# Kernel tuning notes

Hardware: AMD Instinct MI355X
Metric: run time of the kernel (lower is better)

The kernel has to match this reference:

```python
import jax, jax.numpy as jnp
import numpy as np

NEG_INF = float('-inf')

def setup_inputs() -> dict:
    key = jax.random.key(0)
    k1, k2 = jax.random.split(key)
    B, T, S, H, D = 2, 2048, 2048, 8, 64
    q = jax.random.normal(k1, (B, T, H, D), dtype=jnp.float32)
    kv = jax.random.normal(k2, (B, S, 2, H, D), dtype=jnp.float32)
    key_padding_mask = jnp.ones((B, S), dtype=bool)  # True = valid key
    return {"q": q, "kv": kv, "key_padding_mask": key_padding_mask, "causal": 1}


def reference(q, kv, key_padding_mask, causal):
    # q: (B,T,H,D), kv: (B,S,2,H,D)
    k = kv[:, :, 0]  # (B,S,H,D)
    v = kv[:, :, 1]  # (B,S,H,D)
    D = q.shape[-1]
    scale = D ** (-0.5)
    # scores: (B,H,T,S)
    scores = jnp.einsum('bthd,bshd->bhts', q, k) * scale
    # mask: True means "mask out" (matches torch masked_fill semantics)
    mask = ~key_padding_mask[:, None, None, :]  # (B,1,1,S)
    if causal:
        T, S = scores.shape[2], scores.shape[3]
        causal_mask = jnp.triu(jnp.ones((T, S), dtype=bool), k=1)  # (T,S)
        mask = mask | causal_mask[None, None, :, :]
    scores = jnp.where(mask, NEG_INF, scores)
    attn = jax.nn.softmax(scores, axis=-1)
    out = jnp.einsum('bhts,bshd->bthd', attn, v)  # (B,T,H,D)
    return out
```

## Files before the change

### kernel.cpp

```cpp
#include <hip/hip_runtime.h>
#include <hip/hip_bf16.h>

typedef __bf16 bf8_t __attribute__((ext_vector_type(8)));
typedef float  f4_t  __attribute__((ext_vector_type(4)));

constexpr int Bc = 2;
constexpr int Tc = 2048;
constexpr int Sc = 2048;
constexpr int Hc = 8;
constexpr int Dc = 64;
constexpr int BQ = 64;
constexpr int BK = 32;
constexpr int nQB = Tc / BQ;
constexpr int NKT = Sc / BK;
constexpr int NP  = nQB / 2;
constexpr int NS  = 4;
constexpr int TILE_H = 4096;
constexpr int KH = 2048;
constexpr int KTH = 4096;
constexpr int LDP = BK + 4;

__device__ __forceinline__ void g2l16(const void* g, void* l) {
    __builtin_amdgcn_global_load_lds(
        (const __attribute__((address_space(1))) void*)g,
        (__attribute__((address_space(3))) void*)l, 16, 0, 0);
}

__global__ __launch_bounds__(256)
void fa_prep(const float* __restrict__ kv, const int* __restrict__ kpm,
             __bf16* __restrict__ kvb, unsigned* __restrict__ kpmw)
{
    const int idx    = blockIdx.x * 256 + threadIdx.x;
    const int tile   = idx >> 9;
    const int within = idx & 511;
    const int b  = tile >> 9;
    const int h  = (tile >> 6) & 7;
    const int s0 = (tile & 63) * BK;
    __bf16* dst = kvb + (size_t)tile * TILE_H + within * 8;
    bf8_t o;
    if (within < 256) {
        const int row = within >> 3;
        const int col = ((within & 7) * 8) ^ ((row & 7) << 3);
        const float* src = kv + (((size_t)(b * Sc + s0 + row) * 2 + 0) * Hc + h) * Dc + col;
        const float4 x0 = *(const float4*)src;
        const float4 x1 = *(const float4*)(src + 4);
        o[0] = (__bf16)x0.x; o[1] = (__bf16)x0.y; o[2] = (__bf16)x0.z; o[3] = (__bf16)x0.w;
        o[4] = (__bf16)x1.x; o[5] = (__bf16)x1.y; o[6] = (__bf16)x1.z; o[7] = (__bf16)x1.w;
    } else {
        const int c    = within - 256;
        const int vrow = c >> 2;
        const int sc   = (c & 3) * 8;
        const float* src = kv + (((size_t)(b * Sc + s0 + sc) * 2 + 1) * Hc + h) * Dc + vrow;
        #pragma unroll
        for (int j = 0; j < 8; ++j) o[j] = (__bf16)src[(size_t)j * 2 * Hc * Dc];
    }
    *(bf8_t*)dst = o;

    if (idx < Bc * NKT) {
        const int bb = idx >> 6, tt = idx & 63;
        unsigned m = 0;
        for (int k = 0; k < 32; ++k)
            m |= (kpm[bb * Sc + tt * BK + k] != 0 ? 1u : 0u) << k;
        kpmw[idx] = m;
    }
}

__global__ __launch_bounds__(256, 4)
void fa_part(const float* __restrict__ q,
             const __bf16* __restrict__ kvb,
             const unsigned* __restrict__ kpmw,
             const int* __restrict__ causal_p,
             float* __restrict__ part_o,
             float* __restrict__ part_l)
{
    __shared__ __bf16 shK[3 * KTH];
    __shared__ __bf16 Ps[4][16][LDP];

    const int tid  = threadIdx.x;
    const int wave = tid >> 6;
    const int lane = tid & 63;
    const int n16  = lane & 15;
    const int quad = lane >> 4;

    const int bid = blockIdx.x;
    const int h   = bid & 7;
    const int g   = bid >> 3;
    const int b   = g >> 6;
    const int rem = g & 63;
    const int p   = rem >> 2;
    const int s   = rem & 3;
    const int causal = causal_p[0];

    const int nA   = causal ? (nQB - p)  : 32;
    const int nB   = causal ? (p + 1)    : 32;
    const int ntot = nA + nB;
    const int lo   = (ntot * s + 3) >> 2;
    const int hi   = (ntot * (s + 1) + 3) >> 2;

    const __bf16* kvt = kvb + (size_t)((b * Hc + h) * NKT) * TILE_H;
    const unsigned* mw_b = kpmw + b * NKT;

    const int kA_off = n16 * 64 + ((quad * 8) ^ ((n16 & 7) << 3));
    const int lds_st = tid * 8;
    const int vOff   = n16 * 32 + quad * 8;
    const float scale = 0.125f;

    #pragma unroll 1
    for (int seg = 0; seg < 2; ++seg) {
        const int qt = seg ? p : (nQB - 1 - p);
        const int t0 = seg ? (max(lo, nA) - nA) : lo;
        const int t1 = seg ? (hi - nA)          : min(hi, nA);
        if (t0 >= t1) continue;

        __syncthreads();

        const int q_base = qt * BQ;
        const int tq     = q_base + wave * 16 + quad * 4;

        bf8_t a_q[2];
        {
            const int trow = q_base + wave * 16 + n16;
            const float* qrow = q + ((size_t)(b * Tc + trow) * Hc + h) * Dc;
            #pragma unroll
            for (int f = 0; f < 2; ++f) {
                const float4 x0 = *(const float4*)(qrow + f * 32 + quad * 8);
                const float4 x1 = *(const float4*)(qrow + f * 32 + quad * 8 + 4);
                bf8_t v;
                v[0] = (__bf16)(x0.x * scale); v[1] = (__bf16)(x0.y * scale);
                v[2] = (__bf16)(x0.z * scale); v[3] = (__bf16)(x0.w * scale);
                v[4] = (__bf16)(x1.x * scale); v[5] = (__bf16)(x1.y * scale);
                v[6] = (__bf16)(x1.z * scale); v[7] = (__bf16)(x1.w * scale);
                a_q[f] = v;
            }
        }

        f4_t o_acc[4];
        #pragma unroll
        for (int dt = 0; dt < 4; ++dt) o_acc[dt] = (f4_t){0.f, 0.f, 0.f, 0.f};
        float l_r[4] = {0.f, 0.f, 0.f, 0.f};

        int cu = 0, nx = KTH, nn = 2 * KTH;
        {
            const __bf16* src = kvt + (size_t)(2 * t0) * TILE_H;
            g2l16(src + lds_st,          &shK[lds_st]);
            g2l16(src + TILE_H + lds_st, &shK[2048 + lds_st]);
        }

        for (int it = t0; it < t1; ++it) {
            const int kb = it * 64;
            const unsigned cm0 = mw_b[2 * it];
            const unsigned cm1 = mw_b[2 * it + 1];

            const __bf16* vb0 = kvt + (size_t)(2 * it) * TILE_H + KH + vOff;
            const __bf16* vb1 = vb0 + TILE_H;
            const bf8_t bv0 = *(const bf8_t*)(vb0);
            const bf8_t bv1 = *(const bf8_t*)(vb0 + 512);
            const bf8_t bv2 = *(const bf8_t*)(vb0 + 1024);
            const bf8_t bv3 = *(const bf8_t*)(vb0 + 1536);
            const bf8_t bv4 = *(const bf8_t*)(vb1);
            const bf8_t bv5 = *(const bf8_t*)(vb1 + 512);
            const bf8_t bv6 = *(const bf8_t*)(vb1 + 1024);
            const bf8_t bv7 = *(const bf8_t*)(vb1 + 1536);

            if (it + 1 < t1) {
                const __bf16* srcn = kvt + (size_t)(2 * (it + 1)) * TILE_H;
                g2l16(srcn + lds_st,          &shK[nx + lds_st]);
                g2l16(srcn + TILE_H + lds_st, &shK[nx + 2048 + lds_st]);
                asm volatile("s_waitcnt vmcnt(10)" ::: "memory");
            } else {
                asm volatile("s_waitcnt vmcnt(8)" ::: "memory");
            }
            __builtin_amdgcn_s_barrier();

            #pragma unroll
            for (int hh = 0; hh < 2; ++hh) {
                const unsigned cmw = hh ? cm1 : cm0;
                #pragma unroll
                for (int sub = 0; sub < 2; ++sub) {
                    const int kbase = cu + hh * 2048 + sub * 1024;
                    const bf8_t bk0 = *(const bf8_t*)&shK[kbase + kA_off];
                    const bf8_t bk1 = *(const bf8_t*)&shK[kbase + (kA_off ^ 32)];
                    f4_t acc = (f4_t){0.f, 0.f, 0.f, 0.f};
                    __builtin_amdgcn_s_setprio(1);
                    acc = __builtin_amdgcn_mfma_f32_16x16x32_bf16(a_q[0], bk0, acc, 0, 0, 0);
                    acc = __builtin_amdgcn_mfma_f32_16x16x32_bf16(a_q[1], bk1, acc, 0, 0, 0);
                    __builtin_amdgcn_s_setprio(0);
                    const int key = kb + hh * 32 + sub * 16 + n16;
                    const bool kvalid = ((cmw >> (sub * 16 + n16)) & 1u) != 0;
                    #pragma unroll
                    for (int r = 0; r < 4; ++r) {
                        const bool valid = kvalid && (!causal || key <= tq + r);
                        const float pp = valid ? __expf(acc[r] - 8.0f) : 0.0f;
                        l_r[r] += pp;
                        Ps[wave][quad * 4 + r][sub * 16 + n16] = (__bf16)pp;
                    }
                }

                asm volatile("s_waitcnt lgkmcnt(0)" ::: "memory");

                const bf8_t a_p = *(const bf8_t*)&Ps[wave][n16][quad * 8];
                __builtin_amdgcn_s_setprio(1);
                if (hh == 0) {
                    o_acc[0] = __builtin_amdgcn_mfma_f32_16x16x32_bf16(a_p, bv0, o_acc[0], 0, 0, 0);
                    o_acc[1] = __builtin_amdgcn_mfma_f32_16x16x32_bf16(a_p, bv1, o_acc[1], 0, 0, 0);
                    o_acc[2] = __builtin_amdgcn_mfma_f32_16x16x32_bf16(a_p, bv2, o_acc[2], 0, 0, 0);
                    o_acc[3] = __builtin_amdgcn_mfma_f32_16x16x32_bf16(a_p, bv3, o_acc[3], 0, 0, 0);
                } else {
                    o_acc[0] = __builtin_amdgcn_mfma_f32_16x16x32_bf16(a_p, bv4, o_acc[0], 0, 0, 0);
                    o_acc[1] = __builtin_amdgcn_mfma_f32_16x16x32_bf16(a_p, bv5, o_acc[1], 0, 0, 0);
                    o_acc[2] = __builtin_amdgcn_mfma_f32_16x16x32_bf16(a_p, bv6, o_acc[2], 0, 0, 0);
                    o_acc[3] = __builtin_amdgcn_mfma_f32_16x16x32_bf16(a_p, bv7, o_acc[3], 0, 0, 0);
                }
                __builtin_amdgcn_s_setprio(0);
            }

            const int tswap = cu; cu = nx; nx = nn; nn = tswap;
        }

        #pragma unroll
        for (int off = 1; off < 16; off <<= 1) {
            #pragma unroll
            for (int r = 0; r < 4; ++r) l_r[r] += __shfl_xor(l_r[r], off, 16);
        }

        const size_t slot = (size_t)(((b * Hc + h) * NP + p) * NS + s) * 2 + seg;
        float* po = part_o + slot * (BQ * Dc);
        #pragma unroll
        for (int dt = 0; dt < 4; ++dt) {
            #pragma unroll
            for (int r = 0; r < 4; ++r) {
                const int row = wave * 16 + quad * 4 + r;
                po[row * Dc + dt * 16 + n16] = o_acc[dt][r];
            }
        }
        if (n16 == 0) {
            #pragma unroll
            for (int r = 0; r < 4; ++r) {
                const int row = wave * 16 + quad * 4 + r;
                part_l[slot * BQ + row] = l_r[r];
            }
        }
    }
}

__global__ __launch_bounds__(256, 4)
void fa_reduce(const float* __restrict__ part_o,
               const float* __restrict__ part_l,
               const int* __restrict__ causal_p,
               float* __restrict__ out)
{
    const int gtid = blockIdx.x * 256 + threadIdx.x;
    const int e    = gtid & (BQ * Dc / 4 - 1);
    const int qi   = gtid >> 10;
    const int row  = e >> 4;
    const int d4   = e & 15;

    const int qt = qi & (nQB - 1);
    const int h  = (qi >> 5) & (Hc - 1);
    const int b  = qi >> 8;
    const int causal = causal_p[0];

    const int p    = (qt < NP) ? qt : (nQB - 1 - qt);
    const int seg  = (qt < NP) ? 1 : 0;
    const int nA   = causal ? (nQB - p) : 32;
    const int nB   = causal ? (p + 1)   : 32;
    const int ntot = nA + nB;
    const int segLo = seg ? nA : 0;
    const int segHi = seg ? ntot : nA;

    float4 acc = make_float4(0.f, 0.f, 0.f, 0.f);
    float  l   = 0.f;
    #pragma unroll
    for (int s = 0; s < NS; ++s) {
        const int lo = (ntot * s + 3) >> 2;
        const int hi = (ntot * (s + 1) + 3) >> 2;
        if (lo < segHi && segLo < hi) {
            const size_t slot = (size_t)(((b * Hc + h) * NP + p) * NS + s) * 2 + seg;
            const float4 v = *(const float4*)(part_o + slot * (BQ * Dc) + row * Dc + d4 * 4);
            acc.x += v.x; acc.y += v.y; acc.z += v.z; acc.w += v.w;
            l += part_l[slot * BQ + row];
        }
    }
    const float inv = 1.0f / l;
    const int t = qt * BQ + row;
    float4 o;
    o.x = acc.x * inv; o.y = acc.y * inv; o.z = acc.z * inv; o.w = acc.w * inv;
    *(float4*)(out + ((size_t)(b * Tc + t) * Hc + h) * Dc + d4 * 4) = o;
}

extern "C" void kernel_launch(void* const* d_in, const int* in_sizes, int n_in,
                              void* d_out, int out_size, void* d_ws, size_t ws_size,
                              hipStream_t stream) {
    const float* q   = (const float*)d_in[0];
    const float* kv  = (const float*)d_in[1];
    const int*   kpm = (const int*)d_in[2];
    const int*   cz  = (const int*)d_in[3];
    float*       out = (float*)d_out;

    __bf16* kvb = (__bf16*)d_ws;
    const size_t kvb_bytes = (size_t)Bc * Hc * NKT * TILE_H * sizeof(__bf16);
    unsigned* kpmw = (unsigned*)((char*)d_ws + kvb_bytes);
    float* part_o  = (float*)((char*)d_ws + kvb_bytes + 4096);

    const size_t nslots = (size_t)Bc * Hc * NP * NS * 2;
    float* part_l = part_o + nslots * (BQ * Dc);

    const int grid0 = Bc * Hc * NKT * 512 / 256;
    fa_prep<<<grid0, 256, 0, stream>>>(kv, kpm, kvb, kpmw);

    const int grid1 = Bc * Hc * NP * NS;
    fa_part<<<grid1, 256, 0, stream>>>(q, kvb, kpmw, cz, part_o, part_l);

    const int grid2 = (int)((size_t)Bc * Hc * nQB * (BQ * Dc / 4) / 256);
    fa_reduce<<<grid2, 256, 0, stream>>>(part_o, part_l, cz, out);
}
```

Measured before the change: 111.4 us.

## Compute transposed S tile and move P to registers via ds_bpermute instead of LDS

Swaps the MFMA operand order so each lane holds scores for four consecutive keys of a single query row. P is packed to bf16 and rearranged into the A-operand layout with ds_bpermute, replacing the shared-memory Ps round-trip and its lgkmcnt wait. The row-sum reduction becomes per-lane plus cross-quad shuffles and bpermutes. The second half of the V global loads is also moved after the barrier, with the vmcnt thresholds adjusted to match. Split indexing is generalized to NS with division.

```diff
diff --git a/kernel.cpp b/kernel.cpp
--- a/kernel.cpp
+++ b/kernel.cpp
@@ -3,6 +3,7 @@
 
 typedef __bf16 bf8_t __attribute__((ext_vector_type(8)));
 typedef float  f4_t  __attribute__((ext_vector_type(4)));
+typedef int    i4_t  __attribute__((ext_vector_type(4)));
 
 constexpr int Bc = 2;
 constexpr int Tc = 2048;
@@ -18,12 +19,17 @@
 constexpr int TILE_H = 4096;
 constexpr int KH = 2048;
 constexpr int KTH = 4096;
-constexpr int LDP = BK + 4;
 
 __device__ __forceinline__ void g2l16(const void* g, void* l) {
     __builtin_amdgcn_global_load_lds(
         (const __attribute__((address_space(1))) void*)g,
         (__attribute__((address_space(3))) void*)l, 16, 0, 0);
+}
+
+__device__ __forceinline__ int pack_bf16(float lo, float hi) {
+    const unsigned l16 = (unsigned)__builtin_bit_cast(unsigned short, (__bf16)lo);
+    const unsigned h16 = (unsigned)__builtin_bit_cast(unsigned short, (__bf16)hi);
+    return (int)(l16 | (h16 << 16));
 }
 
 __global__ __launch_bounds__(256)
@@ -74,7 +80,6 @@
              float* __restrict__ part_l)
 {
     __shared__ __bf16 shK[3 * KTH];
-    __shared__ __bf16 Ps[4][16][LDP];
 
     const int tid  = threadIdx.x;
     const int wave = tid >> 6;
@@ -85,17 +90,17 @@
     const int bid = blockIdx.x;
     const int h   = bid & 7;
     const int g   = bid >> 3;
-    const int b   = g >> 6;
-    const int rem = g & 63;
-    const int p   = rem >> 2;
-    const int s   = rem & 3;
+    const int b   = g / (NP * NS);
+    const int rem = g % (NP * NS);
+    const int p   = rem / NS;
+    const int s   = rem % NS;
     const int causal = causal_p[0];
 
     const int nA   = causal ? (nQB - p)  : 32;
     const int nB   = causal ? (p + 1)    : 32;
     const int ntot = nA + nB;
-    const int lo   = (ntot * s + 3) >> 2;
-    const int hi   = (ntot * (s + 1) + 3) >> 2;
+    const int lo   = (ntot * s + NS - 1) / NS;
+    const int hi   = (ntot * (s + 1) + NS - 1) / NS;
 
     const __bf16* kvt = kvb + (size_t)((b * Hc + h) * NKT) * TILE_H;
     const unsigned* mw_b = kpmw + b * NKT;
@@ -103,6 +108,9 @@
     const int kA_off = n16 * 64 + ((quad * 8) ^ ((n16 & 7) << 3));
     const int lds_st = tid * 8;
     const int vOff   = n16 * 32 + quad * 8;
+    const int addrA  = (n16 + ((quad & 1) << 5)) << 2;
+    const int addrB  = addrA + 64;
+    const bool hiQ   = quad >= 2;
     const float scale = 0.125f;
 
     #pragma unroll 1
@@ -115,12 +123,11 @@
         __syncthreads();
 
         const int q_base = qt * BQ;
-        const int tq     = q_base + wave * 16 + quad * 4;
+        const int tqn    = q_base + wave * 16 + n16;
 
         bf8_t a_q[2];
         {
-            const int trow = q_base + wave * 16 + n16;
-            const float* qrow = q + ((size_t)(b * Tc + trow) * Hc + h) * Dc;
+            const float* qrow = q + ((size_t)(b * Tc + tqn) * Hc + h) * Dc;
             #pragma unroll
             for (int f = 0; f < 2; ++f) {
                 const float4 x0 = *(const float4*)(qrow + f * 32 + quad * 8);
@@ -137,7 +144,7 @@
         f4_t o_acc[4];
         #pragma unroll
         for (int dt = 0; dt < 4; ++dt) o_acc[dt] = (f4_t){0.f, 0.f, 0.f, 0.f};
-        float l_r[4] = {0.f, 0.f, 0.f, 0.f};
+        float lsum = 0.f;
 
         int cu = 0, nx = KTH, nn = 2 * KTH;
         {
@@ -157,24 +164,26 @@
             const bf8_t bv1 = *(const bf8_t*)(vb0 + 512);
             const bf8_t bv2 = *(const bf8_t*)(vb0 + 1024);
             const bf8_t bv3 = *(const bf8_t*)(vb0 + 1536);
+
+            if (it + 1 < t1) {
+                const __bf16* srcn = kvt + (size_t)(2 * (it + 1)) * TILE_H;
+                g2l16(srcn + lds_st,          &shK[nx + lds_st]);
+                g2l16(srcn + TILE_H + lds_st, &shK[nx + 2048 + lds_st]);
+                asm volatile("s_waitcnt vmcnt(6)" ::: "memory");
+            } else {
+                asm volatile("s_waitcnt vmcnt(4)" ::: "memory");
+            }
+            __builtin_amdgcn_s_barrier();
+
             const bf8_t bv4 = *(const bf8_t*)(vb1);
             const bf8_t bv5 = *(const bf8_t*)(vb1 + 512);
             const bf8_t bv6 = *(const bf8_t*)(vb1 + 1024);
             const bf8_t bv7 = *(const bf8_t*)(vb1 + 1536);
 
-            if (it + 1 < t1) {
-                const __bf16* srcn = kvt + (size_t)(2 * (it + 1)) * TILE_H;
-                g2l16(srcn + lds_st,          &shK[nx + lds_st]);
-                g2l16(srcn + TILE_H + lds_st, &shK[nx + 2048 + lds_st]);
-                asm volatile("s_waitcnt vmcnt(10)" ::: "memory");
-            } else {
-                asm volatile("s_waitcnt vmcnt(8)" ::: "memory");
-            }
-            __builtin_amdgcn_s_barrier();
-
             #pragma unroll
             for (int hh = 0; hh < 2; ++hh) {
                 const unsigned cmw = hh ? cm1 : cm0;
+                int pk[2][2];
                 #pragma unroll
                 for (int sub = 0; sub < 2; ++sub) {
                     const int kbase = cu + hh * 2048 + sub * 1024;
@@ -182,23 +191,38 @@
                     const bf8_t bk1 = *(const bf8_t*)&shK[kbase + (kA_off ^ 32)];
                     f4_t acc = (f4_t){0.f, 0.f, 0.f, 0.f};
                     __builtin_amdgcn_s_setprio(1);
-                    acc = __builtin_amdgcn_mfma_f32_16x16x32_bf16(a_q[0], bk0, acc, 0, 0, 0);
-                    acc = __builtin_amdgcn_mfma_f32_16x16x32_bf16(a_q[1], bk1, acc, 0, 0, 0);
+                    acc = __builtin_amdgcn_mfma_f32_16x16x32_bf16(bk0, a_q[0], acc, 0, 0, 0);
+                    acc = __builtin_amdgcn_mfma_f32_16x16x32_bf16(bk1, a_q[1], acc, 0, 0, 0);
                     __builtin_amdgcn_s_setprio(0);
-                    const int key = kb + hh * 32 + sub * 16 + n16;
-                    const bool kvalid = ((cmw >> (sub * 16 + n16)) & 1u) != 0;
+                    const int keyb = kb + hh * 32 + sub * 16 + quad * 4;
+                    const unsigned mb = cmw >> (sub * 16 + quad * 4);
+                    float pv[4];
                     #pragma unroll
                     for (int r = 0; r < 4; ++r) {
-                        const bool valid = kvalid && (!causal || key <= tq + r);
+                        const bool valid = ((mb >> r) & 1u) && (!causal || keyb + r <= tqn);
                         const float pp = valid ? __expf(acc[r] - 8.0f) : 0.0f;
-                        l_r[r] += pp;
-                        Ps[wave][quad * 4 + r][sub * 16 + n16] = (__bf16)pp;
+                        lsum += pp;
+                        pv[r] = pp;
                     }
+                    pk[sub][0] = pack_bf16(pv[0], pv[1]);
+                    pk[sub][1] = pack_bf16(pv[2], pv[3]);
                 }
 
-                asm volatile("s_waitcnt lgkmcnt(0)" ::: "memory");
-
-                const bf8_t a_p = *(const bf8_t*)&Ps[wave][n16][quad * 8];
+                const int a0 = __builtin_amdgcn_ds_bpermute(addrA, pk[0][0]);
+                const int a1 = __builtin_amdgcn_ds_bpermute(addrA, pk[0][1]);
+                const int b0 = __builtin_amdgcn_ds_bpermute(addrB, pk[0][0]);
+                const int b1 = __builtin_amdgcn_ds_bpermute(addrB, pk[0][1]);
+                const int c0 = __builtin_amdgcn_ds_bpermute(addrA, pk[1][0]);
+                const int c1 = __builtin_amdgcn_ds_bpermute(addrA, pk[1][1]);
+                const int d0 = __builtin_amdgcn_ds_bpermute(addrB, pk[1][0]);
+                const int d1 = __builtin_amdgcn_ds_bpermute(addrB, pk[1][1]);
+                union { i4_t i; bf8_t b; } u;
+                u.i[0] = hiQ ? c0 : a0;
+                u.i[1] = hiQ ? c1 : a1;
+                u.i[2] = hiQ ? d0 : b0;
+                u.i[3] = hiQ ? d1 : b1;
+                const bf8_t a_p = u.b;
+
                 __builtin_amdgcn_s_setprio(1);
                 if (hh == 0) {
                     o_acc[0] = __builtin_amdgcn_mfma_f32_16x16x32_bf16(a_p, bv0, o_acc[0], 0, 0, 0);
@@ -217,10 +241,14 @@
             const int tswap = cu; cu = nx; nx = nn; nn = tswap;
         }
 
+        lsum += __shfl_xor(lsum, 16);
+        lsum += __shfl_xor(lsum, 32);
+        float l_row[4];
         #pragma unroll
-        for (int off = 1; off < 16; off <<= 1) {
-            #pragma unroll
-            for (int r = 0; r < 4; ++r) l_r[r] += __shfl_xor(l_r[r], off, 16);
+        for (int r = 0; r < 4; ++r) {
+            const int li = __builtin_amdgcn_ds_bpermute((quad * 4 + r) << 2,
+                                                        __builtin_bit_cast(int, lsum));
+            l_row[r] = __builtin_bit_cast(float, li);
         }
 
         const size_t slot = (size_t)(((b * Hc + h) * NP + p) * NS + s) * 2 + seg;
@@ -237,7 +265,7 @@
             #pragma unroll
             for (int r = 0; r < 4; ++r) {
                 const int row = wave * 16 + quad * 4 + r;
-                part_l[slot * BQ + row] = l_r[r];
+                part_l[slot * BQ + row] = l_row[r];
             }
         }
     }
@@ -272,9 +300,9 @@
     float  l   = 0.f;
     #pragma unroll
     for (int s = 0; s < NS; ++s) {
-        const int lo = (ntot * s + 3) >> 2;
-        const int hi = (ntot * (s + 1) + 3) >> 2;
-        if (lo < segHi && segLo < hi) {
+        const int lo = (ntot * s + NS - 1) / NS;
+        const int hi = (ntot * (s + 1) + NS - 1) / NS;
+        if (lo < segHi && segLo < hi && lo < hi) {
             const size_t slot = (size_t)(((b * Hc + h) * NP + p) * NS + s) * 2 + seg;
             const float4 v = *(const float4*)(part_o + slot * (BQ * Dc) + row * Dc + d4 * 4);
             acc.x += v.x; acc.y += v.y; acc.z += v.z; acc.w += v.w;
```

Result: slower. 114.1 us (+2.5%).
